# Kernel tuning notes

Measured on AMD Instinct MI355X. Metric: run time of the kernel, lower is better.

The kernel has to match this reference:

```python
import jax, jax.numpy as jnp
import numpy as np

EPS = 1e-5

def _layer_norm(x, w):
    mu = jnp.mean(x, axis=-1, keepdims=True)
    var = jnp.mean(jnp.square(x - mu), axis=-1, keepdims=True)
    return (x - mu) * jax.lax.rsqrt(var + EPS) * w

def setup_inputs() -> dict:
    key = jax.random.key(0)
    ks = jax.random.split(key, 5)
    B, T, C, H = 2, 2048, 1024, 16
    std = 0.02
    return {
        "x": jax.random.normal(ks[0], (B, T, C), dtype=jnp.float32),
        "ln1_w": jnp.ones((C,), dtype=jnp.float32),
        "w_attn": jax.random.normal(ks[1], (C, 3 * C), dtype=jnp.float32) * std,
        "w_proj": jax.random.normal(ks[2], (C, C), dtype=jnp.float32) * std,
        "ln2_w": jnp.ones((C,), dtype=jnp.float32),
        "w_fc": jax.random.normal(ks[3], (C, 4 * C), dtype=jnp.float32) * std,
        "w_cproj": jax.random.normal(ks[4], (4 * C, C), dtype=jnp.float32) * std,
    }

def reference(x, ln1_w, w_attn, w_proj, ln2_w, w_fc, w_cproj):
    B, T, C = x.shape
    H = 16
    Dh = C // H
    # --- causal self-attention on ln1(x) ---
    h = _layer_norm(x, ln1_w)
    qkv = h @ w_attn                      # [B,T,3C]
    q, k, v = jnp.split(qkv, 3, axis=-1)
    # [B,T,C] -> [B,H,T,Dh]
    q = q.reshape(B, T, H, Dh).transpose(0, 2, 1, 3)
    k = k.reshape(B, T, H, Dh).transpose(0, 2, 1, 3)
    v = v.reshape(B, T, H, Dh).transpose(0, 2, 1, 3)
    # NOTE: original scales by full embed dim C**-0.5, not head_dim**-0.5
    scores = jnp.einsum('bhqd,bhkd->bhqk', q, k) * (C ** -0.5)
    causal = jnp.tril(jnp.ones((T, T), dtype=bool))
    scores = jnp.where(causal, scores, -jnp.inf)
    probs = jax.nn.softmax(scores, axis=-1)  # dropout=0.0 (eval)
    y = jnp.einsum('bhqk,bhkd->bhqd', probs, v)
    y = y.transpose(0, 2, 1, 3).reshape(B, T, C)
    x = x + y @ w_proj
    # --- MLP on ln2(x) ---
    h = _layer_norm(x, ln2_w)
    x = x + jax.nn.relu(h @ w_fc) @ w_cproj
    return x
```

## Files before the change

kernel.cpp:

```cpp
#include <hip/hip_runtime.h>

typedef __attribute__((ext_vector_type(8))) __bf16 bf16x8;
typedef __attribute__((ext_vector_type(4))) float f32x4;
typedef __attribute__((ext_vector_type(8))) unsigned short u16x8;
typedef __attribute__((ext_vector_type(4))) unsigned short u16x4;
typedef unsigned short u16;

__device__ __forceinline__ u16 f2bf(float f) {
  return __builtin_bit_cast(u16, (__bf16)f);
}
__device__ __forceinline__ float bf2f(u16 u) {
  return __builtin_bit_cast(float, ((unsigned)u) << 16);
}

__device__ __forceinline__ f32x4 mfma16(bf16x8 a, bf16x8 b, f32x4 c) {
  return __builtin_amdgcn_mfma_f32_16x16x32_bf16(a, b, c, 0, 0, 0);
}

__device__ __forceinline__ void gl_lds16(const void* g, void* l) {
  __builtin_amdgcn_global_load_lds(
      (const __attribute__((address_space(1))) unsigned int*)g,
      (__attribute__((address_space(3))) unsigned int*)l, 16, 0, 0);
}

__device__ __forceinline__ f32x4 fmax4(f32x4 a, f32x4 b) {
  f32x4 r;
  r[0] = fmaxf(a[0], b[0]); r[1] = fmaxf(a[1], b[1]);
  r[2] = fmaxf(a[2], b[2]); r[3] = fmaxf(a[3], b[3]);
  return r;
}

__global__ __launch_bounds__(256) void convT(const float* __restrict__ in,
                                             u16* __restrict__ outT, int K, int N) {
  __shared__ float tile[64][65];
  const int t = threadIdx.x;
  const int tk = blockIdx.x * 64, tn = blockIdx.y * 64;
  const int lk = t >> 4, ln = (t & 15) * 4;
#pragma unroll
  for (int r = 0; r < 4; ++r) {
    const int k = lk + r * 16;
    const float4 v = *(const float4*)(in + (size_t)(tk + k) * N + tn + ln);
    tile[k][ln + 0] = v.x; tile[k][ln + 1] = v.y;
    tile[k][ln + 2] = v.z; tile[k][ln + 3] = v.w;
  }
  __syncthreads();
  const int sn = t >> 2, sk = (t & 3) * 4;
#pragma unroll
  for (int j = 0; j < 4; ++j) {
    const int k = sk + j * 16;
    ushort4 o;
    o.x = f2bf(tile[k + 0][sn]); o.y = f2bf(tile[k + 1][sn]);
    o.z = f2bf(tile[k + 2][sn]); o.w = f2bf(tile[k + 3][sn]);
    *(ushort4*)(outT + (size_t)(tn + sn) * K + tk + k) = o;
  }
}

__global__ __launch_bounds__(256) void vtrans(const u16* __restrict__ qkvb,
                                              u16* __restrict__ vT) {
  __shared__ u16 tile[64][72];
  const int t = threadIdx.x;
  const int tt0 = blockIdx.x * 64;
  const int bh = blockIdx.y;
  const int b = bh >> 4, h = bh & 15;
  const u16* src = qkvb + (size_t)(b * 2048 + tt0) * 3072 + 2048 + h * 64;
  {
    const int tl = t >> 2, d0 = (t & 3) * 16;
    const u16x8 a0 = *(const u16x8*)(src + (size_t)tl * 3072 + d0);
    const u16x8 a1 = *(const u16x8*)(src + (size_t)tl * 3072 + d0 + 8);
    *(u16x8*)(&tile[tl][d0]) = a0;
    *(u16x8*)(&tile[tl][d0 + 8]) = a1;
  }
  __syncthreads();
  {
    const int dh = t >> 2, t0 = (t & 3) * 16;
    u16x8 o0, o1;
#pragma unroll
    for (int jj = 0; jj < 8; ++jj) {
      o0[jj] = tile[t0 + jj][dh];
      o1[jj] = tile[t0 + 8 + jj][dh];
    }
    u16* dst = vT + ((size_t)bh * 64 + dh) * 2048 + tt0 + t0;
    *(u16x8*)dst = o0;
    *(u16x8*)(dst + 8) = o1;
  }
}

__global__ __launch_bounds__(256) void ln_bf16(const float* __restrict__ x,
                                               const float* __restrict__ wgt,
                                               u16* __restrict__ out) {
  const int row = blockIdx.x, t = threadIdx.x;
  const float4 v = ((const float4*)(x + (size_t)row * 1024))[t];
  float s = v.x + v.y + v.z + v.w;
  float q = v.x * v.x + v.y * v.y + v.z * v.z + v.w * v.w;
#pragma unroll
  for (int d = 32; d; d >>= 1) { s += __shfl_xor(s, d); q += __shfl_xor(q, d); }
  __shared__ float sb[8];
  const int wv = t >> 6;
  if ((t & 63) == 0) { sb[wv] = s; sb[4 + wv] = q; }
  __syncthreads();
  s = sb[0] + sb[1] + sb[2] + sb[3];
  q = sb[4] + sb[5] + sb[6] + sb[7];
  const float mu = s * (1.f / 1024.f);
  const float rstd = rsqrtf(q * (1.f / 1024.f) - mu * mu + 1e-5f);
  const float4 w4 = ((const float4*)wgt)[t];
  ushort4 o;
  o.x = f2bf((v.x - mu) * rstd * w4.x);
  o.y = f2bf((v.y - mu) * rstd * w4.y);
  o.z = f2bf((v.z - mu) * rstd * w4.z);
  o.w = f2bf((v.w - mu) * rstd * w4.w);
  *(ushort4*)(out + (size_t)row * 1024 + t * 4) = o;
}

__global__ __launch_bounds__(256) void reduce_ln(const float* __restrict__ x,
                                                 const u16* __restrict__ p, int nseg,
                                                 const float* __restrict__ wgt,
                                                 float* __restrict__ x1,
                                                 u16* __restrict__ h2) {
  const int row = blockIdx.x, t = threadIdx.x;
  const size_t ro = (size_t)row * 1024 + t * 4;
  float4 v = *(const float4*)(x + ro);
  for (int sgm = 0; sgm < nseg; ++sgm) {
    const ushort4 u = *(const ushort4*)(p + (size_t)sgm * 4096 * 1024 + ro);
    v.x += bf2f(u.x); v.y += bf2f(u.y); v.z += bf2f(u.z); v.w += bf2f(u.w);
  }
  *(float4*)(x1 + ro) = v;
  float s = v.x + v.y + v.z + v.w;
  float q = v.x * v.x + v.y * v.y + v.z * v.z + v.w * v.w;
#pragma unroll
  for (int d = 32; d; d >>= 1) { s += __shfl_xor(s, d); q += __shfl_xor(q, d); }
  __shared__ float sb[8];
  const int wv = t >> 6;
  if ((t & 63) == 0) { sb[wv] = s; sb[4 + wv] = q; }
  __syncthreads();
  s = sb[0] + sb[1] + sb[2] + sb[3];
  q = sb[4] + sb[5] + sb[6] + sb[7];
  const float mu = s * (1.f / 1024.f);
  const float rstd = rsqrtf(q * (1.f / 1024.f) - mu * mu + 1e-5f);
  const float4 w4 = ((const float4*)wgt)[t];
  ushort4 o;
  o.x = f2bf((v.x - mu) * rstd * w4.x);
  o.y = f2bf((v.y - mu) * rstd * w4.y);
  o.z = f2bf((v.z - mu) * rstd * w4.z);
  o.w = f2bf((v.w - mu) * rstd * w4.w);
  *(ushort4*)(h2 + ro) = o;
}

__global__ __launch_bounds__(256) void reduce_out(const float* __restrict__ x1,
                                                  const u16* __restrict__ p, int nseg,
                                                  float* __restrict__ out) {
  const int i = blockIdx.x * blockDim.x + threadIdx.x;
  const size_t ro = (size_t)i * 4;
  float4 v = *(const float4*)(x1 + ro);
  for (int sgm = 0; sgm < nseg; ++sgm) {
    const ushort4 u = *(const ushort4*)(p + (size_t)sgm * 4096 * 1024 + ro);
    v.x += bf2f(u.x); v.y += bf2f(u.y); v.z += bf2f(u.z); v.w += bf2f(u.w);
  }
  *(float4*)(out + ro) = v;
}

template <int EPI>
__global__ __launch_bounds__(256) void gemm128(const u16* __restrict__ A,
                                               const u16* __restrict__ Bt,
                                               void* __restrict__ outp,
                                               int M, int N, int K) {
  __shared__ u16 As[2][4096];
  __shared__ u16 Bs[2][4096];
  const unsigned gx = gridDim.x, gy = gridDim.y, gxy = gx * gy;
  const unsigned nwg = gxy * gridDim.z;
  unsigned f = (blockIdx.z * gy + blockIdx.y) * gx + blockIdx.x;
  if ((nwg & 7u) == 0u) { const unsigned qq = nwg >> 3; f = (f & 7u) * qq + (f >> 3); }
  const int bx = f % gx, by = (f / gx) % gy, bz = f / gxy;

  const int t = threadIdx.x, w = t >> 6, l = t & 63;
  const int lr = l & 15, g = l >> 4;
  const int row0 = by * 128, col0 = bx * 128;
  const int segK = K / gridDim.z;
  const int k0 = bz * segK, kend = k0 + segK;
  const int wr = w >> 1, wc = w & 1;
  f32x4 acc[4][4] = {};

  const int sr = t >> 2;
  const int sk = (((t & 3) ^ (sr & 3)) << 3);
  const u16* Ag = A + (size_t)(row0 + sr) * K + sk;
  const u16* Bg = Bt + (size_t)(col0 + sr) * K + sk;
  const size_t rstride = (size_t)64 * K;

  auto stage = [&](int kt, int bb) {
    u16* AsW = As[bb] + w * 512;
    u16* BsW = Bs[bb] + w * 512;
    gl_lds16(Ag + kt, AsW);
    gl_lds16(Ag + kt + rstride, AsW + 2048);
    gl_lds16(Bg + kt, BsW);
    gl_lds16(Bg + kt + rstride, BsW + 2048);
  };

  const int gsw = (g ^ (lr & 3)) * 8;

  stage(k0, 0);
  __syncthreads();
  int cur = 0;
  for (int kt = k0; kt < kend; kt += 32) {
    if (kt + 32 < kend) stage(kt + 32, cur ^ 1);
    bf16x8 af[4], bfr[4];
#pragma unroll
    for (int m = 0; m < 4; ++m)
      af[m] = *(const bf16x8*)(As[cur] + (wr * 64 + m * 16 + lr) * 32 + gsw);
#pragma unroll
    for (int n = 0; n < 4; ++n)
      bfr[n] = *(const bf16x8*)(Bs[cur] + (wc * 64 + n * 16 + lr) * 32 + gsw);
#pragma unroll
    for (int m = 0; m < 4; ++m)
#pragma unroll
      for (int n = 0; n < 4; ++n) acc[m][n] = mfma16(af[m], bfr[n], acc[m][n]);
    __syncthreads();
    cur ^= 1;
  }

  const size_t segoff = (size_t)bz * M * N;
#pragma unroll
  for (int m = 0; m < 4; ++m)
#pragma unroll
    for (int n = 0; n < 4; ++n)
#pragma unroll
      for (int r = 0; r < 4; ++r) {
        const int row = row0 + wr * 64 + m * 16 + g * 4 + r;
        const int col = col0 + wc * 64 + n * 16 + lr;
        const size_t idx = (size_t)row * N + col;
        const float v = acc[m][n][r];
        if constexpr (EPI == 0) ((u16*)outp)[idx] = f2bf(v);
        else if constexpr (EPI == 2) ((u16*)outp)[idx] = f2bf(fmaxf(v, 0.f));
        else ((u16*)outp)[segoff + idx] = f2bf(v);
      }
}

__global__ __launch_bounds__(256) void attn_fwd(const u16* __restrict__ qkvb,
                                                const u16* __restrict__ vT,
                                                u16* __restrict__ y) {
  __shared__ u16 Ks[2][4096];
  __shared__ u16 Vs[2][4096];
  __shared__ u16 Pb[4][16 * 72];
  const int t = threadIdx.x, w = t >> 6, l = t & 63;
  const int lr = l & 15, g = l >> 4;
  const unsigned f = blockIdx.y * gridDim.x + blockIdx.x;
  const int xcd = f & 7, j = f >> 3;
  const int bh = xcd + 8 * (j & 3);
  const int qt = 31 - (j >> 2);
  const int b = bh >> 4, h = bh & 15;
  const size_t base = (size_t)b * 2048 * 3072;
  const u16* Kg = qkvb + base + 1024 + h * 64;
  const u16* Vg = vT + (size_t)bh * 64 * 2048;
  u16* Pw = &Pb[w][0];
  const float SCL = 0.0450842200277855f;

  auto stageK = [&](int kv0, int bb) {
#pragma unroll
    for (int r = 0; r < 2; ++r) {
      const int dl = (r * 256 + t) * 16;
      const int row = dl >> 7;
      const int srcb = (dl & 127) ^ ((row & 7) << 4);
      gl_lds16(Kg + (size_t)(kv0 + row) * 3072 + (srcb >> 1),
               (char*)Ks[bb] + r * 4096 + w * 1024);
    }
  };
  auto stageV = [&](int kv0, int bb) {
#pragma unroll
    for (int r = 0; r < 2; ++r) {
      const int dl = (r * 256 + t) * 16;
      const int dh = dl >> 7;
      const int srcb = (dl & 127) ^ ((dh & 7) << 4);
      gl_lds16(Vg + (size_t)dh * 2048 + kv0 + (srcb >> 1),
               (char*)Vs[bb] + r * 4096 + w * 1024);
    }
  };

  const int q0w = qt * 64 + w * 16, nt = qt + 1;
  const u16* Qp = qkvb + base + (size_t)(q0w + lr) * 3072 + h * 64;
  const bf16x8 qf0 = *(const bf16x8*)(Qp + g * 8);
  const bf16x8 qf1 = *(const bf16x8*)(Qp + 32 + g * 8);
  f32x4 o[4] = {};
  float m1 = -1e30f, s1 = 0.f;

  stageK(0, 0);
  stageV(0, 0);
  __syncthreads();

  int ct = 0;
  for (int tt = 0; tt < nt; ++tt) {
    const int kv0 = tt * 64;
    if (tt + 1 < nt) {
      stageK(kv0 + 64, ct ^ 1);
      stageV(kv0 + 64, ct ^ 1);
    }

    const u16* Kbuf = Ks[ct];
    const u16* Vbuf = Vs[ct];
    f32x4 s4[4];
#pragma unroll
    for (int i = 0; i < 4; ++i) {
      const int row = i * 16 + lr;
      const int sw = (row & 7) << 4;
      const bf16x8 k0 = *(const bf16x8*)(Kbuf + row * 64 + (((g * 16) ^ sw) >> 1));
      const bf16x8 k1 = *(const bf16x8*)(Kbuf + row * 64 + (((64 + g * 16) ^ sw) >> 1));
      f32x4 z = {0.f, 0.f, 0.f, 0.f};
      z = mfma16(k0, qf0, z);
      z = mfma16(k1, qf1, z);
      s4[i] = z * SCL;
    }
    if (kv0 + 64 > q0w) {
#pragma unroll
      for (int i = 0; i < 4; ++i)
#pragma unroll
        for (int r = 0; r < 4; ++r)
          if (kv0 + i * 16 + g * 4 + r > q0w + lr) s4[i][r] = -1e30f;
    }
    const f32x4 mm = fmax4(fmax4(s4[0], s4[1]), fmax4(s4[2], s4[3]));
    float mx = fmaxf(fmaxf(mm[0], mm[1]), fmaxf(mm[2], mm[3]));
    mx = fmaxf(mx, __shfl_xor(mx, 16));
    mx = fmaxf(mx, __shfl_xor(mx, 32));
    if (!__all(mx <= m1 + 8.f)) {
      const float mn = fmaxf(m1, mx);
      const float sc = exp2f(m1 - mn);
      m1 = mn;
      s1 *= sc;
      float scr[4];
#pragma unroll
      for (int r = 0; r < 4; ++r) scr[r] = __shfl(sc, g * 4 + r);
#pragma unroll
      for (int n = 0; n < 4; ++n)
#pragma unroll
        for (int r = 0; r < 4; ++r) o[n][r] *= scr[r];
    }
    float ps = 0.f;
#pragma unroll
    for (int i = 0; i < 4; ++i) {
      u16x4 pk;
#pragma unroll
      for (int r = 0; r < 4; ++r) {
        const float p = exp2f(s4[i][r] - m1);
        ps += p;
        pk[r] = f2bf(p);
      }
      *(u16x4*)(Pw + lr * 72 + i * 16 + g * 4) = pk;
    }
    s1 += ps;
#pragma unroll
    for (int s = 0; s < 2; ++s) {
      const bf16x8 pa = *(const bf16x8*)(Pw + lr * 72 + s * 32 + g * 8);
#pragma unroll
      for (int n = 0; n < 4; ++n) {
        const int dh = n * 16 + lr;
        const bf16x8 vf = *(const bf16x8*)(
            Vbuf + dh * 64 + (((s * 64 + g * 16) ^ ((dh & 7) << 4)) >> 1));
        o[n] = mfma16(pa, vf, o[n]);
      }
    }
    __syncthreads();
    ct ^= 1;
  }

  float den = s1;
  den += __shfl_xor(den, 16);
  den += __shfl_xor(den, 32);
  const float iv = 1.f / den;
  float ivr[4];
#pragma unroll
  for (int r = 0; r < 4; ++r) ivr[r] = __shfl(iv, g * 4 + r);
#pragma unroll
  for (int n = 0; n < 4; ++n)
#pragma unroll
    for (int r = 0; r < 4; ++r) {
      const int row = q0w + g * 4 + r;
      const int col = h * 64 + n * 16 + lr;
      y[(size_t)(b * 2048 + row) * 1024 + col] = f2bf(o[n][r] * ivr[r]);
    }
}

extern "C" void kernel_launch(void* const* d_in, const int* in_sizes, int n_in,
                              void* d_out, int out_size, void* d_ws, size_t ws_size,
                              hipStream_t stream) {
  const float* x      = (const float*)d_in[0];
  const float* ln1w   = (const float*)d_in[1];
  const float* wattn  = (const float*)d_in[2];
  const float* wproj  = (const float*)d_in[3];
  const float* ln2w   = (const float*)d_in[4];
  const float* wfc    = (const float*)d_in[5];
  const float* wcproj = (const float*)d_in[6];
  float* out = (float*)d_out;
  char* ws = (char*)d_ws;
  const size_t MB = 1024 * 1024;
  u16* qkvb    = (u16*)(ws + 0);
  u16* cprojP  = (u16*)(ws + 0);
  u16* h1      = (u16*)(ws + 24 * MB);
  u16* yb      = (u16*)(ws + 24 * MB);
  u16* projP   = (u16*)(ws + 32 * MB);
  float* x1    = (float*)(ws + 48 * MB);
  u16* h2      = (u16*)(ws + 64 * MB);
  u16* vT      = (u16*)(ws + 72 * MB);
  u16* hf      = (u16*)(ws + 72 * MB);
  u16* wattnT  = (u16*)(ws + 104 * MB);
  u16* wprojT  = (u16*)(ws + 110 * MB);
  u16* wcprojT = (u16*)(ws + 104 * MB);
  u16* wfcT    = (u16*)(ws + 112 * MB);

  convT<<<dim3(16, 48), 256, 0, stream>>>(wattn, wattnT, 1024, 3072);
  convT<<<dim3(16, 16), 256, 0, stream>>>(wproj, wprojT, 1024, 1024);
  convT<<<dim3(16, 64), 256, 0, stream>>>(wfc, wfcT, 1024, 4096);

  ln_bf16<<<4096, 256, 0, stream>>>(x, ln1w, h1);
  gemm128<0><<<dim3(24, 32, 1), 256, 0, stream>>>(h1, wattnT, qkvb, 4096, 3072, 1024);
  vtrans<<<dim3(32, 32), 256, 0, stream>>>(qkvb, vT);
  attn_fwd<<<dim3(32, 32), 256, 0, stream>>>(qkvb, vT, yb);
  gemm128<4><<<dim3(8, 32, 2), 256, 0, stream>>>(yb, wprojT, projP, 4096, 1024, 1024);
  convT<<<dim3(64, 16), 256, 0, stream>>>(wcproj, wcprojT, 4096, 1024);
  reduce_ln<<<4096, 256, 0, stream>>>(x, projP, 2, ln2w, x1, h2);
  gemm128<2><<<dim3(32, 32, 1), 256, 0, stream>>>(h2, wfcT, hf, 4096, 4096, 1024);
  gemm128<4><<<dim3(8, 32, 4), 256, 0, stream>>>(hf, wcprojT, cprojP, 4096, 1024, 4096);
  reduce_out<<<4096, 256, 0, stream>>>(x1, cprojP, 4, out);
}
```

Before: 253.9 us.

## Add 256x256-tile 8-wave GEMM with fine-grained prefetch for MLP fc layer

Replaces the 128x128 GEMM for the fc+ReLU layer (4096x4096x1024) with a new 256x256 tile kernel using 512 threads, split half-tile staging interleaved with MFMA sub-steps, setprio around compute, and XCD-aware block remapping. Larger tiles raise arithmetic intensity and LDS reuse. The grid shrinks to 256 workgroups, roughly one per CU, which risks load imbalance or tail effects. LDS use is 128KB per block, so occupancy drops despite the launch bound.

```diff
diff --git a/kernel.cpp b/kernel.cpp
--- a/kernel.cpp
+++ b/kernel.cpp
@@ -230,6 +230,86 @@
         if constexpr (EPI == 0) ((u16*)outp)[idx] = f2bf(v);
         else if constexpr (EPI == 2) ((u16*)outp)[idx] = f2bf(fmaxf(v, 0.f));
         else ((u16*)outp)[segoff + idx] = f2bf(v);
+      }
+}
+
+__global__ __launch_bounds__(512, 2) void gemm256_relu(const u16* __restrict__ A,
+                                                       const u16* __restrict__ Bt,
+                                                       u16* __restrict__ outp,
+                                                       int M, int N, int K) {
+  __shared__ u16 S[2][32768];
+  const unsigned gx = gridDim.x;
+  const unsigned nwg = gx * gridDim.y;
+  unsigned f = blockIdx.y * gx + blockIdx.x;
+  if ((nwg & 7u) == 0u) { const unsigned qq = nwg >> 3; f = (f & 7u) * qq + (f >> 3); }
+  const int bx = f % gx, by = f / gx;
+  const int t = threadIdx.x, w = t >> 6, l = t & 63;
+  const int lr = l & 15, g = l >> 4;
+  const int wr = w >> 2, wc = w & 3;
+  const int row0 = by * 256, col0 = bx * 256;
+  const int NT = K >> 6;
+
+  f32x4 acc[8][4] = {};
+
+  const int jr0 = t >> 2, jk0 = (t & 3) << 3;
+  const int jr1 = (t + 512) >> 2, jk1 = (t & 3) << 3;
+  auto stage_half = [&](int ht, int idx) {
+    const int buf = ht & 1;
+    u16* db = &S[buf][(idx & 1) * 16384 + (idx >> 1) * 8192 + w * 512];
+    const u16* gb = (idx & 1) ? Bt : A;
+    const int rc0 = (idx & 1) ? col0 : row0;
+    const int kb = ht * 64 + (idx >> 1) * 32;
+    gl_lds16(gb + (size_t)(rc0 + jr0) * K + kb + jk0, db);
+    gl_lds16(gb + (size_t)(rc0 + jr1) * K + kb + jk1, db + 4096);
+  };
+
+  stage_half(0, 0); stage_half(0, 1); stage_half(0, 2); stage_half(0, 3);
+  stage_half(1, 0); stage_half(1, 1);
+  asm volatile("s_waitcnt vmcnt(4)" ::: "memory");
+  __builtin_amdgcn_s_barrier();
+
+  for (int T = 0; T < NT; ++T) {
+    const int cur = T & 1;
+    const u16* Ab = &S[cur][0];
+    const u16* Bb = &S[cur][16384];
+    bf16x8 bfr[4];
+#pragma unroll
+    for (int sub = 0; sub < 4; ++sub) {
+      const int mq = sub & 1, ks = sub >> 1;
+      if (mq == 0) {
+#pragma unroll
+        for (int n = 0; n < 4; ++n)
+          bfr[n] = *(const bf16x8*)(Bb + ks * 8192 + (wc * 64 + n * 16 + lr) * 32 + g * 8);
+      }
+      bf16x8 af[4];
+#pragma unroll
+      for (int m = 0; m < 4; ++m)
+        af[m] = *(const bf16x8*)(Ab + ks * 8192 +
+                                 (wr * 128 + mq * 64 + m * 16 + lr) * 32 + g * 8);
+      if (sub < 2) { if (T + 1 < NT) stage_half(T + 1, 2 + sub); }
+      else         { if (T + 2 < NT) stage_half(T + 2, sub - 2); }
+      __builtin_amdgcn_s_barrier();
+      __builtin_amdgcn_s_setprio(1);
+#pragma unroll
+      for (int m = 0; m < 4; ++m)
+#pragma unroll
+        for (int n = 0; n < 4; ++n)
+          acc[mq * 4 + m][n] = mfma16(af[m], bfr[n], acc[mq * 4 + m][n]);
+      __builtin_amdgcn_s_setprio(0);
+      if (sub == 3) asm volatile("s_waitcnt vmcnt(4)" ::: "memory");
+      __builtin_amdgcn_s_barrier();
+    }
+  }
+
+#pragma unroll
+  for (int m = 0; m < 8; ++m)
+#pragma unroll
+    for (int n = 0; n < 4; ++n)
+#pragma unroll
+      for (int r = 0; r < 4; ++r) {
+        const int row = row0 + wr * 128 + m * 16 + g * 4 + r;
+        const int col = col0 + wc * 64 + n * 16 + lr;
+        outp[(size_t)row * N + col] = f2bf(fmaxf(acc[m][n][r], 0.f));
       }
 }
 
@@ -413,7 +493,7 @@
   gemm128<4><<<dim3(8, 32, 2), 256, 0, stream>>>(yb, wprojT, projP, 4096, 1024, 1024);
   convT<<<dim3(64, 16), 256, 0, stream>>>(wcproj, wcprojT, 4096, 1024);
   reduce_ln<<<4096, 256, 0, stream>>>(x, projP, 2, ln2w, x1, h2);
-  gemm128<2><<<dim3(32, 32, 1), 256, 0, stream>>>(h2, wfcT, hf, 4096, 4096, 1024);
+  gemm256_relu<<<dim3(16, 16), 512, 0, stream>>>(h2, wfcT, hf, 4096, 4096, 1024);
   gemm128<4><<<dim3(8, 32, 4), 256, 0, stream>>>(hf, wcprojT, cprojP, 4096, 1024, 4096);
   reduce_out<<<4096, 256, 0, stream>>>(x1, cprojP, 4, out);
 }
```

Result: faster. 241.0 us (-5.1%).
